# Optimization experiments

Hardware: AMD Instinct MI355X
Metric: run time of the kernel (lower is better)

Reference implementation:

```python
import jax, jax.numpy as jnp
import numpy as np

N_NODES = 50000
N_EDGES = 800000
NFEAT, NHID, NTOPIC = 256, 128, 64


def setup_inputs() -> dict:
    key = jax.random.key(0)
    k1, k2, k3, k4 = jax.random.split(key, 4)
    x = jax.random.normal(k1, (N_NODES, NFEAT), dtype=jnp.float32)
    edge_index = jax.random.randint(k2, (2, N_EDGES), 0, N_NODES, dtype=jnp.int64)
    W1 = jax.random.normal(k3, (NFEAT, NHID), dtype=jnp.float32) * (1.0 / np.sqrt(NFEAT))
    b1 = jnp.zeros((NHID,), dtype=jnp.float32)
    W2 = jax.random.normal(k4, (NHID, NTOPIC), dtype=jnp.float32) * (1.0 / np.sqrt(NHID))
    b2 = jnp.zeros((NTOPIC,), dtype=jnp.float32)
    return {"x": x, "edge_index": edge_index, "W1": W1, "b1": b1, "W2": W2, "b2": b2}


def reference(x, edge_index, W1, b1, W2, b2):
    # GCNConv (add_self_loops=False): symmetric normalization computed once (cached=True)
    n = x.shape[0]
    src, dst = edge_index[0], edge_index[1]
    deg = jnp.zeros((n,), dtype=x.dtype).at[dst].add(1.0)  # in-degree at targets
    deg_inv_sqrt = jnp.where(deg > 0, jax.lax.rsqrt(jnp.maximum(deg, 1.0)), 0.0)
    norm = deg_inv_sqrt[src] * deg_inv_sqrt[dst]  # [E]

    def gcn_conv(h, W, b):
        h = h @ W                                    # dense linear (bias=False)
        msg = norm[:, None] * h[src]                 # [E, out] edge messages
        agg = jax.ops.segment_sum(msg, dst, num_segments=n)
        return agg + b

    h = jax.nn.relu(gcn_conv(x, W1, b1))
    # dropout is identity in eval mode (train=False)
    return gcn_conv(h, W2, b2)
```

## Files before the change

kernel.cpp:

```cpp
#include <hip/hip_runtime.h>
#include <stdint.h>

#define NFEAT 256
#define NHID 128
#define NTOPIC 64
#define CAP 64

typedef __attribute__((ext_vector_type(8))) short bf16x8;
typedef __attribute__((ext_vector_type(4))) float f32x4;

__device__ inline float bf2f(unsigned int u16) {
    union { unsigned int i; float f; } v; v.i = u16 << 16; return v.f;
}
__device__ inline unsigned short f2bf(float f) {
    union { float f; unsigned int i; } v; v.f = f;
    unsigned int r = v.i + 0x7fff + ((v.i >> 16) & 1);
    return (unsigned short)(r >> 16);
}

__global__ void warm_kernel(const uint4* __restrict__ p, int total16) {
    int stride = gridDim.x * blockDim.x;
    unsigned acc = 0;
    for (int i = blockIdx.x * blockDim.x + threadIdx.x; i < total16; i += stride) {
        uint4 v = p[i];
        acc ^= v.x ^ v.y ^ v.z ^ v.w;
    }
    asm volatile("" :: "v"(acc));
}

__global__ void bucket_kernel(const int* __restrict__ src, const int* __restrict__ dst,
                              int* __restrict__ cnt, int* __restrict__ esrc_p, int E) {
    int e = blockIdx.x * blockDim.x + threadIdx.x;
    if (e < E) {
        int s = src[e], d = dst[e];
        int pos = atomicAdd(&cnt[d], 1);
        if (pos < CAP) esrc_p[(size_t)d * CAP + pos] = s;
    }
}

__global__ void castx_kernel(const float4* __restrict__ x4, const int* __restrict__ cnt,
                             ushort4* __restrict__ xb4, int total4) {
    int stride = gridDim.x * blockDim.x;
    for (int i = blockIdx.x * blockDim.x + threadIdx.x; i < total4; i += stride) {
        int c = cnt[i >> 6];
        float dn = (c > 0) ? rsqrtf((float)c) : 0.0f;
        float4 v = x4[i];
        ushort4 o;
        o.x = f2bf(dn * v.x); o.y = f2bf(dn * v.y);
        o.z = f2bf(dn * v.z); o.w = f2bf(dn * v.w);
        xb4[i] = o;
    }
}

__global__ void tw_kernel(const float* __restrict__ W, unsigned short* __restrict__ Wt,
                          int K, int N) {
    int idx = blockIdx.x * blockDim.x + threadIdx.x;
    if (idx < K * N) {
        int k = idx / N, c = idx - k * N;
        Wt[c * K + k] = f2bf(W[idx]);
    }
}

__global__ __launch_bounds__(256) void gemm1_mfma(const unsigned short* __restrict__ xb,
                                                  const unsigned short* __restrict__ Wt1,
                                                  unsigned short* __restrict__ h, int n) {
    int node0 = blockIdx.x * 16;
    int wave = threadIdx.x >> 6;
    int lane = threadIdx.x & 63;
    int r = lane & 15;
    int g = lane >> 4;
    int col0 = wave * 32;

    const unsigned short* arow  = xb  + (size_t)(node0 + r) * 256 + g * 8;
    const unsigned short* brow0 = Wt1 + (size_t)(col0 + r) * 256 + g * 8;
    const unsigned short* brow1 = Wt1 + (size_t)(col0 + 16 + r) * 256 + g * 8;

    f32x4 acc0 = {0.f, 0.f, 0.f, 0.f};
    f32x4 acc1 = {0.f, 0.f, 0.f, 0.f};
    #pragma unroll
    for (int k0 = 0; k0 < 256; k0 += 32) {
        bf16x8 a  = *(const bf16x8*)(arow + k0);
        bf16x8 b0 = *(const bf16x8*)(brow0 + k0);
        bf16x8 b1 = *(const bf16x8*)(brow1 + k0);
        acc0 = __builtin_amdgcn_mfma_f32_16x16x32_bf16(a, b0, acc0, 0, 0, 0);
        acc1 = __builtin_amdgcn_mfma_f32_16x16x32_bf16(a, b1, acc1, 0, 0, 0);
    }
    #pragma unroll
    for (int i = 0; i < 4; ++i) {
        int node = node0 + g * 4 + i;
        h[(size_t)node * 128 + col0 + r]      = f2bf(acc0[i]);
        h[(size_t)node * 128 + col0 + 16 + r] = f2bf(acc1[i]);
    }
}

__global__ __launch_bounds__(256) void gemm2_mfma(const unsigned short* __restrict__ agg1,
                                                  const unsigned short* __restrict__ Wt2,
                                                  unsigned short* __restrict__ h2, int n) {
    int node0 = blockIdx.x * 16;
    int wave = threadIdx.x >> 6;
    int lane = threadIdx.x & 63;
    int r = lane & 15;
    int g = lane >> 4;
    int col0 = wave * 16;

    const unsigned short* arow = agg1 + (size_t)(node0 + r) * 128 + g * 8;
    const unsigned short* brow = Wt2  + (size_t)(col0 + r) * 128 + g * 8;

    f32x4 acc = {0.f, 0.f, 0.f, 0.f};
    #pragma unroll
    for (int k0 = 0; k0 < 128; k0 += 32) {
        bf16x8 a = *(const bf16x8*)(arow + k0);
        bf16x8 b = *(const bf16x8*)(brow + k0);
        acc = __builtin_amdgcn_mfma_f32_16x16x32_bf16(a, b, acc, 0, 0, 0);
    }
    #pragma unroll
    for (int i = 0; i < 4; ++i) {
        int node = node0 + g * 4 + i;
        h2[(size_t)node * 64 + col0 + r] = f2bf(acc[i]);
    }
}

__global__ __launch_bounds__(256) void agg1_kernel(const int* __restrict__ cnt,
                                                   const int* __restrict__ esrc_p,
                                                   const unsigned short* __restrict__ h,
                                                   const float* __restrict__ bias,
                                                   unsigned short* __restrict__ agg, int n) {
    int wave = threadIdx.x >> 6;
    int lane = threadIdx.x & 63;
    int node = blockIdx.x * 4 + wave;
    if (node >= n) return;
    int c = cnt[node];
    float disn = (c > 0) ? rsqrtf((float)c) : 0.0f;
    int cntn = min(c, CAP);
    int g = lane >> 4;
    int r = lane & 15;
    const int* row = esrc_p + (size_t)node * CAP;
    const uint4* h4 = (const uint4*)h;

    float acc[8] = {0.f,0.f,0.f,0.f,0.f,0.f,0.f,0.f};
    for (int j = 0; j < cntn; j += 4) {
        int jj = j + g;
        if (jj < cntn) {
            int s = row[jj];
            uint4 hv = h4[(size_t)s * 16 + r];
            acc[0] += bf2f(hv.x & 0xffff); acc[1] += bf2f(hv.x >> 16);
            acc[2] += bf2f(hv.y & 0xffff); acc[3] += bf2f(hv.y >> 16);
            acc[4] += bf2f(hv.z & 0xffff); acc[5] += bf2f(hv.z >> 16);
            acc[6] += bf2f(hv.w & 0xffff); acc[7] += bf2f(hv.w >> 16);
        }
    }
    #pragma unroll
    for (int i = 0; i < 8; ++i) {
        acc[i] += __shfl_xor(acc[i], 16);
        acc[i] += __shfl_xor(acc[i], 32);
    }
    if (g == 0) {
        float4 b0 = ((const float4*)bias)[r * 2];
        float4 b1 = ((const float4*)bias)[r * 2 + 1];
        uint4 o;
        o.x = (unsigned)f2bf(disn * fmaxf(disn * acc[0] + b0.x, 0.f)) |
              ((unsigned)f2bf(disn * fmaxf(disn * acc[1] + b0.y, 0.f)) << 16);
        o.y = (unsigned)f2bf(disn * fmaxf(disn * acc[2] + b0.z, 0.f)) |
              ((unsigned)f2bf(disn * fmaxf(disn * acc[3] + b0.w, 0.f)) << 16);
        o.z = (unsigned)f2bf(disn * fmaxf(disn * acc[4] + b1.x, 0.f)) |
              ((unsigned)f2bf(disn * fmaxf(disn * acc[5] + b1.y, 0.f)) << 16);
        o.w = (unsigned)f2bf(disn * fmaxf(disn * acc[6] + b1.z, 0.f)) |
              ((unsigned)f2bf(disn * fmaxf(disn * acc[7] + b1.w, 0.f)) << 16);
        ((uint4*)agg)[(size_t)node * 16 + r] = o;
    }
}

__global__ __launch_bounds__(256) void agg2_kernel(const int* __restrict__ cnt,
                                                   const int* __restrict__ esrc_p,
                                                   const unsigned short* __restrict__ h2,
                                                   const float* __restrict__ bias,
                                                   float* __restrict__ out, int n) {
    int wave = threadIdx.x >> 6;
    int lane = threadIdx.x & 63;
    int node = blockIdx.x * 4 + wave;
    if (node >= n) return;
    int c = cnt[node];
    float disn = (c > 0) ? rsqrtf((float)c) : 0.0f;
    int cntn = min(c, CAP);
    int g = lane >> 4;
    int r = lane & 15;
    const int* row = esrc_p + (size_t)node * CAP;
    const uint2* h2v = (const uint2*)h2;

    float acc[4] = {0.f,0.f,0.f,0.f};
    for (int j = 0; j < cntn; j += 4) {
        int jj = j + g;
        if (jj < cntn) {
            int s = row[jj];
            uint2 hv = h2v[(size_t)s * 16 + r];
            acc[0] += bf2f(hv.x & 0xffff); acc[1] += bf2f(hv.x >> 16);
            acc[2] += bf2f(hv.y & 0xffff); acc[3] += bf2f(hv.y >> 16);
        }
    }
    #pragma unroll
    for (int i = 0; i < 4; ++i) {
        acc[i] += __shfl_xor(acc[i], 16);
        acc[i] += __shfl_xor(acc[i], 32);
    }
    if (g == 0) {
        float4 b = ((const float4*)bias)[r];
        float4 o;
        o.x = disn * acc[0] + b.x; o.y = disn * acc[1] + b.y;
        o.z = disn * acc[2] + b.z; o.w = disn * acc[3] + b.w;
        ((float4*)out)[(size_t)node * 16 + r] = o;
    }
}

extern "C" void kernel_launch(void* const* d_in, const int* in_sizes, int n_in,
                              void* d_out, int out_size, void* d_ws, size_t ws_size,
                              hipStream_t stream) {
    const float* x  = (const float*)d_in[0];
    const int*   ei = (const int*)d_in[1];
    const float* W1 = (const float*)d_in[2];
    const float* b1 = (const float*)d_in[3];
    const float* W2 = (const float*)d_in[4];
    const float* b2 = (const float*)d_in[5];
    float* out = (float*)d_out;

    const int n = in_sizes[0] / NFEAT;
    const int E = in_sizes[1] / 2;
    const int* src = ei;
    const int* dst = ei + E;

    const int n_al = (n + 63) & ~63;

    uintptr_t p = (uintptr_t)d_ws;
    auto take = [&p](size_t bytes) { uintptr_t r = p; p = (p + bytes + 15) & ~(uintptr_t)15; return r; };
    int*   esrc_p = (int*)take((size_t)n * CAP * 4);
    int*   cnt    = (int*)take((size_t)n_al * 4);
    unsigned short* Wt1  = (unsigned short*)take((size_t)NHID * NFEAT * 2);
    unsigned short* Wt2  = (unsigned short*)take((size_t)NTOPIC * NHID * 2);
    unsigned short* xb   = (unsigned short*)take((size_t)n * NFEAT * 2);
    unsigned short* h    = (unsigned short*)take((size_t)n * NHID * 2);
    unsigned short* agg1 = (unsigned short*)take((size_t)n * NHID * 2);

    hipMemsetAsync(cnt, 0, (size_t)n * sizeof(int), stream);
    warm_kernel<<<2048, 256, 0, stream>>>((const uint4*)esrc_p, n * CAP / 4);
    bucket_kernel<<<(E + 255) / 256, 256, 0, stream>>>(src, dst, cnt, esrc_p, E);

    castx_kernel<<<2048, 256, 0, stream>>>((const float4*)x, cnt, (ushort4*)xb, n * NFEAT / 4);
    tw_kernel<<<(NFEAT * NHID + 255) / 256, 256, 0, stream>>>(W1, Wt1, NFEAT, NHID);
    tw_kernel<<<(NHID * NTOPIC + 255) / 256, 256, 0, stream>>>(W2, Wt2, NHID, NTOPIC);

    gemm1_mfma<<<n / 16, 256, 0, stream>>>(xb, Wt1, h, n);
    agg1_kernel<<<(n + 3) / 4, 256, 0, stream>>>(cnt, esrc_p, h, b1, agg1, n);

    gemm2_mfma<<<n / 16, 256, 0, stream>>>(agg1, Wt2, h, n);
    agg2_kernel<<<(n + 3) / 4, 256, 0, stream>>>(cnt, esrc_p, h, b2, out, n);
}
```

Measured before the change: 272.6 us.

## Build padded adjacency via binned two-pass sort and fuse x cast into GEMM1

Replaces per-node global atomics with a bin histogram, scan, scatter into bins of 128 nodes, and a per-bin LDS pass that writes the padded adjacency with coalesced stores. Source indices are stored as 16-bit values, which halves adjacency traffic in the aggregation kernels. The separate cast-to-bf16 kernel and its buffer are removed; GEMM1 now reads fp32 x directly and scales and converts it in registers. In exchange this adds several launches and depends on node ids fitting in 16 bits (true for 50000 nodes).

```diff
diff --git a/kernel.cpp b/kernel.cpp
--- a/kernel.cpp
+++ b/kernel.cpp
@@ -5,6 +5,8 @@
 #define NHID 128
 #define NTOPIC 64
 #define CAP 64
+#define NPB 128
+#define NPB_SHIFT 7
 
 typedef __attribute__((ext_vector_type(8))) short bf16x8;
 typedef __attribute__((ext_vector_type(4))) float f32x4;
@@ -18,38 +20,73 @@
     return (unsigned short)(r >> 16);
 }
 
-__global__ void warm_kernel(const uint4* __restrict__ p, int total16) {
-    int stride = gridDim.x * blockDim.x;
-    unsigned acc = 0;
-    for (int i = blockIdx.x * blockDim.x + threadIdx.x; i < total16; i += stride) {
-        uint4 v = p[i];
-        acc ^= v.x ^ v.y ^ v.z ^ v.w;
-    }
-    asm volatile("" :: "v"(acc));
-}
-
-__global__ void bucket_kernel(const int* __restrict__ src, const int* __restrict__ dst,
-                              int* __restrict__ cnt, int* __restrict__ esrc_p, int E) {
+__global__ __launch_bounds__(256) void hist_kernel(const int* __restrict__ dst,
+                                                   int* __restrict__ binCnt, int E, int NB) {
+    __shared__ int lcnt[512];
+    for (int i = threadIdx.x; i < NB; i += 256) lcnt[i] = 0;
+    __syncthreads();
+    int stride = gridDim.x * 256;
+    for (int e = blockIdx.x * 256 + threadIdx.x; e < E; e += stride)
+        atomicAdd(&lcnt[dst[e] >> NPB_SHIFT], 1);
+    __syncthreads();
+    for (int i = threadIdx.x; i < NB; i += 256)
+        if (lcnt[i]) atomicAdd(&binCnt[i], lcnt[i]);
+}
+
+__global__ __launch_bounds__(512) void binscan_kernel(const int* __restrict__ binCnt,
+                                                      int* __restrict__ binptr,
+                                                      int* __restrict__ bincur, int NB) {
+    __shared__ int s[512];
+    int t = threadIdx.x;
+    s[t] = (t < NB) ? binCnt[t] : 0;
+    __syncthreads();
+    for (int off = 1; off < 512; off <<= 1) {
+        int v = (t >= off) ? s[t - off] : 0;
+        __syncthreads();
+        s[t] += v;
+        __syncthreads();
+    }
+    if (t < NB) {
+        int base = (t == 0) ? 0 : s[t - 1];
+        binptr[t] = base;
+        bincur[t] = base;
+        if (t == NB - 1) binptr[NB] = s[t];
+    }
+}
+
+__global__ void binscatter_kernel(const int* __restrict__ src, const int* __restrict__ dst,
+                                  int* __restrict__ bincur, unsigned* __restrict__ rec, int E) {
     int e = blockIdx.x * blockDim.x + threadIdx.x;
     if (e < E) {
-        int s = src[e], d = dst[e];
-        int pos = atomicAdd(&cnt[d], 1);
-        if (pos < CAP) esrc_p[(size_t)d * CAP + pos] = s;
-    }
-}
-
-__global__ void castx_kernel(const float4* __restrict__ x4, const int* __restrict__ cnt,
-                             ushort4* __restrict__ xb4, int total4) {
-    int stride = gridDim.x * blockDim.x;
-    for (int i = blockIdx.x * blockDim.x + threadIdx.x; i < total4; i += stride) {
-        int c = cnt[i >> 6];
-        float dn = (c > 0) ? rsqrtf((float)c) : 0.0f;
-        float4 v = x4[i];
-        ushort4 o;
-        o.x = f2bf(dn * v.x); o.y = f2bf(dn * v.y);
-        o.z = f2bf(dn * v.z); o.w = f2bf(dn * v.w);
-        xb4[i] = o;
-    }
+        int d = dst[e];
+        int b = d >> NPB_SHIFT;
+        int pos = atomicAdd(&bincur[b], 1);
+        rec[pos] = (unsigned)src[e] | ((unsigned)(d & (NPB - 1)) << 16);
+    }
+}
+
+__global__ __launch_bounds__(256) void csrbuild_kernel(const unsigned* __restrict__ rec,
+                                                       const int* __restrict__ binptr,
+                                                       unsigned short* __restrict__ esrc_p,
+                                                       int* __restrict__ cnt, int NB) {
+    __shared__ unsigned short lcsr[NPB * CAP];
+    __shared__ int lcnt[NPB];
+    int b = blockIdx.x;
+    for (int i = threadIdx.x; i < NPB; i += 256) lcnt[i] = 0;
+    __syncthreads();
+    int beg = binptr[b], end = binptr[b + 1];
+    for (int i = beg + threadIdx.x; i < end; i += 256) {
+        unsigned r = rec[i];
+        int dl = r >> 16;
+        int pos = atomicAdd(&lcnt[dl], 1);
+        if (pos < CAP) lcsr[dl * CAP + pos] = (unsigned short)(r & 0xffff);
+    }
+    __syncthreads();
+    uint4* gout = (uint4*)(esrc_p + (size_t)b * NPB * CAP);
+    const uint4* lin = (const uint4*)lcsr;
+    for (int i = threadIdx.x; i < NPB * CAP * 2 / 16; i += 256) gout[i] = lin[i];
+    int node0 = b * NPB;
+    for (int i = threadIdx.x; i < NPB; i += 256) cnt[node0 + i] = lcnt[i];
 }
 
 __global__ void tw_kernel(const float* __restrict__ W, unsigned short* __restrict__ Wt,
@@ -61,7 +98,8 @@
     }
 }
 
-__global__ __launch_bounds__(256) void gemm1_mfma(const unsigned short* __restrict__ xb,
+__global__ __launch_bounds__(256) void gemm1_mfma(const float* __restrict__ x,
+                                                  const int* __restrict__ cnt,
                                                   const unsigned short* __restrict__ Wt1,
                                                   unsigned short* __restrict__ h, int n) {
     int node0 = blockIdx.x * 16;
@@ -70,8 +108,11 @@
     int r = lane & 15;
     int g = lane >> 4;
     int col0 = wave * 32;
-
-    const unsigned short* arow  = xb  + (size_t)(node0 + r) * 256 + g * 8;
+    int row = node0 + r;
+
+    int c = cnt[row];
+    float dn = (c > 0) ? rsqrtf((float)c) : 0.0f;
+    const float* arow = x + (size_t)row * 256 + g * 8;
     const unsigned short* brow0 = Wt1 + (size_t)(col0 + r) * 256 + g * 8;
     const unsigned short* brow1 = Wt1 + (size_t)(col0 + 16 + r) * 256 + g * 8;
 
@@ -79,7 +120,13 @@
     f32x4 acc1 = {0.f, 0.f, 0.f, 0.f};
     #pragma unroll
     for (int k0 = 0; k0 < 256; k0 += 32) {
-        bf16x8 a  = *(const bf16x8*)(arow + k0);
+        float4 v0 = *(const float4*)(arow + k0);
+        float4 v1 = *(const float4*)(arow + k0 + 4);
+        bf16x8 a;
+        a[0] = (short)f2bf(dn * v0.x); a[1] = (short)f2bf(dn * v0.y);
+        a[2] = (short)f2bf(dn * v0.z); a[3] = (short)f2bf(dn * v0.w);
+        a[4] = (short)f2bf(dn * v1.x); a[5] = (short)f2bf(dn * v1.y);
+        a[6] = (short)f2bf(dn * v1.z); a[7] = (short)f2bf(dn * v1.w);
         bf16x8 b0 = *(const bf16x8*)(brow0 + k0);
         bf16x8 b1 = *(const bf16x8*)(brow1 + k0);
         acc0 = __builtin_amdgcn_mfma_f32_16x16x32_bf16(a, b0, acc0, 0, 0, 0);
@@ -121,7 +168,7 @@
 }
 
 __global__ __launch_bounds__(256) void agg1_kernel(const int* __restrict__ cnt,
-                                                   const int* __restrict__ esrc_p,
+                                                   const unsigned short* __restrict__ esrc_p,
                                                    const unsigned short* __restrict__ h,
                                                    const float* __restrict__ bias,
                                                    unsigned short* __restrict__ agg, int n) {
@@ -134,7 +181,7 @@
     int cntn = min(c, CAP);
     int g = lane >> 4;
     int r = lane & 15;
-    const int* row = esrc_p + (size_t)node * CAP;
+    const unsigned short* row = esrc_p + (size_t)node * CAP;
     const uint4* h4 = (const uint4*)h;
 
     float acc[8] = {0.f,0.f,0.f,0.f,0.f,0.f,0.f,0.f};
@@ -171,7 +218,7 @@
 }
 
 __global__ __launch_bounds__(256) void agg2_kernel(const int* __restrict__ cnt,
-                                                   const int* __restrict__ esrc_p,
+                                                   const unsigned short* __restrict__ esrc_p,
                                                    const unsigned short* __restrict__ h2,
                                                    const float* __restrict__ bias,
                                                    float* __restrict__ out, int n) {
@@ -184,7 +231,7 @@
     int cntn = min(c, CAP);
     int g = lane >> 4;
     int r = lane & 15;
-    const int* row = esrc_p + (size_t)node * CAP;
+    const unsigned short* row = esrc_p + (size_t)node * CAP;
     const uint2* h2v = (const uint2*)h2;
 
     float acc[4] = {0.f,0.f,0.f,0.f};
@@ -227,27 +274,32 @@
     const int* src = ei;
     const int* dst = ei + E;
 
-    const int n_al = (n + 63) & ~63;
+    const int NB = (n + NPB - 1) / NPB;
+    const int n_pad = NB * NPB;
 
     uintptr_t p = (uintptr_t)d_ws;
     auto take = [&p](size_t bytes) { uintptr_t r = p; p = (p + bytes + 15) & ~(uintptr_t)15; return r; };
-    int*   esrc_p = (int*)take((size_t)n * CAP * 4);
-    int*   cnt    = (int*)take((size_t)n_al * 4);
+    unsigned short* esrc_p = (unsigned short*)take((size_t)n_pad * CAP * 2);
+    unsigned* rec  = (unsigned*)take((size_t)E * 4);
+    int* cnt    = (int*)take((size_t)n_pad * 4);
+    int* binCnt = (int*)take((size_t)(NB + 1) * 4);
+    int* binptr = (int*)take((size_t)(NB + 1) * 4);
+    int* bincur = (int*)take((size_t)(NB + 1) * 4);
     unsigned short* Wt1  = (unsigned short*)take((size_t)NHID * NFEAT * 2);
     unsigned short* Wt2  = (unsigned short*)take((size_t)NTOPIC * NHID * 2);
-    unsigned short* xb   = (unsigned short*)take((size_t)n * NFEAT * 2);
     unsigned short* h    = (unsigned short*)take((size_t)n * NHID * 2);
     unsigned short* agg1 = (unsigned short*)take((size_t)n * NHID * 2);
 
-    hipMemsetAsync(cnt, 0, (size_t)n * sizeof(int), stream);
-    warm_kernel<<<2048, 256, 0, stream>>>((const uint4*)esrc_p, n * CAP / 4);
-    bucket_kernel<<<(E + 255) / 256, 256, 0, stream>>>(src, dst, cnt, esrc_p, E);
-
-    castx_kernel<<<2048, 256, 0, stream>>>((const float4*)x, cnt, (ushort4*)xb, n * NFEAT / 4);
+    hipMemsetAsync(binCnt, 0, (size_t)(NB + 1) * sizeof(int), stream);
+    hist_kernel<<<512, 256, 0, stream>>>(dst, binCnt, E, NB);
+    binscan_kernel<<<1, 512, 0, stream>>>(binCnt, binptr, bincur, NB);
+    binscatter_kernel<<<(E + 255) / 256, 256, 0, stream>>>(src, dst, bincur, rec, E);
+    csrbuild_kernel<<<NB, 256, 0, stream>>>(rec, binptr, esrc_p, cnt, NB);
+
     tw_kernel<<<(NFEAT * NHID + 255) / 256, 256, 0, stream>>>(W1, Wt1, NFEAT, NHID);
     tw_kernel<<<(NHID * NTOPIC + 255) / 256, 256, 0, stream>>>(W2, Wt2, NHID, NTOPIC);
 
-    gemm1_mfma<<<n / 16, 256, 0, stream>>>(xb, Wt1, h, n);
+    gemm1_mfma<<<n / 16, 256, 0, stream>>>(x, cnt, Wt1, h, n);
     agg1_kernel<<<(n + 3) / 4, 256, 0, stream>>>(cnt, esrc_p, h, b1, agg1, n);
 
     gemm2_mfma<<<n / 16, 256, 0, stream>>>(agg1, Wt2, h, n);
```

After: 537.4 us. 1.97x slower.

## Fuse x cast into GEMM1, pack edge indices as 16-bit, unroll gathers

Applied to the files above, without the earlier changes.

The separate castx pass is removed. GEMM1 now reads fp32 x directly and applies the degree scaling and bf16 conversion in registers, which avoids writing and re-reading a bf16 copy of x. Bucketed source indices are stored as 16-bit values packed with atomicOr into a zeroed buffer. This halves the index footprint read by both aggregation kernels and drops the warm-up kernel, at the cost of an extra memset and atomic ORs, and it only works while the node count fits in 16 bits. The aggregation loops now process two neighbour slots per iteration to raise memory-level parallelism.

```diff
diff --git a/kernel.cpp b/kernel.cpp
--- a/kernel.cpp
+++ b/kernel.cpp
@@ -18,37 +18,14 @@
     return (unsigned short)(r >> 16);
 }
 
-__global__ void warm_kernel(const uint4* __restrict__ p, int total16) {
-    int stride = gridDim.x * blockDim.x;
-    unsigned acc = 0;
-    for (int i = blockIdx.x * blockDim.x + threadIdx.x; i < total16; i += stride) {
-        uint4 v = p[i];
-        acc ^= v.x ^ v.y ^ v.z ^ v.w;
-    }
-    asm volatile("" :: "v"(acc));
-}
-
 __global__ void bucket_kernel(const int* __restrict__ src, const int* __restrict__ dst,
-                              int* __restrict__ cnt, int* __restrict__ esrc_p, int E) {
+                              int* __restrict__ cnt, unsigned* __restrict__ esrc_w, int E) {
     int e = blockIdx.x * blockDim.x + threadIdx.x;
     if (e < E) {
         int s = src[e], d = dst[e];
         int pos = atomicAdd(&cnt[d], 1);
-        if (pos < CAP) esrc_p[(size_t)d * CAP + pos] = s;
-    }
-}
-
-__global__ void castx_kernel(const float4* __restrict__ x4, const int* __restrict__ cnt,
-                             ushort4* __restrict__ xb4, int total4) {
-    int stride = gridDim.x * blockDim.x;
-    for (int i = blockIdx.x * blockDim.x + threadIdx.x; i < total4; i += stride) {
-        int c = cnt[i >> 6];
-        float dn = (c > 0) ? rsqrtf((float)c) : 0.0f;
-        float4 v = x4[i];
-        ushort4 o;
-        o.x = f2bf(dn * v.x); o.y = f2bf(dn * v.y);
-        o.z = f2bf(dn * v.z); o.w = f2bf(dn * v.w);
-        xb4[i] = o;
+        if (pos < CAP)
+            atomicOr(&esrc_w[d * (CAP / 2) + (pos >> 1)], ((unsigned)s) << ((pos & 1) * 16));
     }
 }
 
@@ -61,7 +38,8 @@
     }
 }
 
-__global__ __launch_bounds__(256) void gemm1_mfma(const unsigned short* __restrict__ xb,
+__global__ __launch_bounds__(256) void gemm1_mfma(const float* __restrict__ x,
+                                                  const int* __restrict__ cnt,
                                                   const unsigned short* __restrict__ Wt1,
                                                   unsigned short* __restrict__ h, int n) {
     int node0 = blockIdx.x * 16;
@@ -70,8 +48,11 @@
     int r = lane & 15;
     int g = lane >> 4;
     int col0 = wave * 32;
-
-    const unsigned short* arow  = xb  + (size_t)(node0 + r) * 256 + g * 8;
+    int row = node0 + r;
+
+    int c = cnt[row];
+    float dn = (c > 0) ? rsqrtf((float)c) : 0.0f;
+    const float* arow = x + (size_t)row * 256 + g * 8;
     const unsigned short* brow0 = Wt1 + (size_t)(col0 + r) * 256 + g * 8;
     const unsigned short* brow1 = Wt1 + (size_t)(col0 + 16 + r) * 256 + g * 8;
 
@@ -79,7 +60,13 @@
     f32x4 acc1 = {0.f, 0.f, 0.f, 0.f};
     #pragma unroll
     for (int k0 = 0; k0 < 256; k0 += 32) {
-        bf16x8 a  = *(const bf16x8*)(arow + k0);
+        float4 v0 = *(const float4*)(arow + k0);
+        float4 v1 = *(const float4*)(arow + k0 + 4);
+        bf16x8 a;
+        a[0] = (short)f2bf(dn * v0.x); a[1] = (short)f2bf(dn * v0.y);
+        a[2] = (short)f2bf(dn * v0.z); a[3] = (short)f2bf(dn * v0.w);
+        a[4] = (short)f2bf(dn * v1.x); a[5] = (short)f2bf(dn * v1.y);
+        a[6] = (short)f2bf(dn * v1.z); a[7] = (short)f2bf(dn * v1.w);
         bf16x8 b0 = *(const bf16x8*)(brow0 + k0);
         bf16x8 b1 = *(const bf16x8*)(brow1 + k0);
         acc0 = __builtin_amdgcn_mfma_f32_16x16x32_bf16(a, b0, acc0, 0, 0, 0);
@@ -121,7 +108,7 @@
 }
 
 __global__ __launch_bounds__(256) void agg1_kernel(const int* __restrict__ cnt,
-                                                   const int* __restrict__ esrc_p,
+                                                   const unsigned short* __restrict__ esrc_p,
                                                    const unsigned short* __restrict__ h,
                                                    const float* __restrict__ bias,
                                                    unsigned short* __restrict__ agg, int n) {
@@ -134,14 +121,23 @@
     int cntn = min(c, CAP);
     int g = lane >> 4;
     int r = lane & 15;
-    const int* row = esrc_p + (size_t)node * CAP;
+    const unsigned short* row = esrc_p + (size_t)node * CAP;
     const uint4* h4 = (const uint4*)h;
 
     float acc[8] = {0.f,0.f,0.f,0.f,0.f,0.f,0.f,0.f};
-    for (int j = 0; j < cntn; j += 4) {
-        int jj = j + g;
-        if (jj < cntn) {
-            int s = row[jj];
+    for (int j = 0; j < cntn; j += 8) {
+        int jj0 = j + g;
+        int jj1 = j + 4 + g;
+        if (jj0 < cntn) {
+            int s = row[jj0];
+            uint4 hv = h4[(size_t)s * 16 + r];
+            acc[0] += bf2f(hv.x & 0xffff); acc[1] += bf2f(hv.x >> 16);
+            acc[2] += bf2f(hv.y & 0xffff); acc[3] += bf2f(hv.y >> 16);
+            acc[4] += bf2f(hv.z & 0xffff); acc[5] += bf2f(hv.z >> 16);
+            acc[6] += bf2f(hv.w & 0xffff); acc[7] += bf2f(hv.w >> 16);
+        }
+        if (jj1 < cntn) {
+            int s = row[jj1];
             uint4 hv = h4[(size_t)s * 16 + r];
             acc[0] += bf2f(hv.x & 0xffff); acc[1] += bf2f(hv.x >> 16);
             acc[2] += bf2f(hv.y & 0xffff); acc[3] += bf2f(hv.y >> 16);
@@ -171,7 +167,7 @@
 }
 
 __global__ __launch_bounds__(256) void agg2_kernel(const int* __restrict__ cnt,
-                                                   const int* __restrict__ esrc_p,
+                                                   const unsigned short* __restrict__ esrc_p,
                                                    const unsigned short* __restrict__ h2,
                                                    const float* __restrict__ bias,
                                                    float* __restrict__ out, int n) {
@@ -184,14 +180,21 @@
     int cntn = min(c, CAP);
     int g = lane >> 4;
     int r = lane & 15;
-    const int* row = esrc_p + (size_t)node * CAP;
+    const unsigned short* row = esrc_p + (size_t)node * CAP;
     const uint2* h2v = (const uint2*)h2;
 
     float acc[4] = {0.f,0.f,0.f,0.f};
-    for (int j = 0; j < cntn; j += 4) {
-        int jj = j + g;
-        if (jj < cntn) {
-            int s = row[jj];
+    for (int j = 0; j < cntn; j += 8) {
+        int jj0 = j + g;
+        int jj1 = j + 4 + g;
+        if (jj0 < cntn) {
+            int s = row[jj0];
+            uint2 hv = h2v[(size_t)s * 16 + r];
+            acc[0] += bf2f(hv.x & 0xffff); acc[1] += bf2f(hv.x >> 16);
+            acc[2] += bf2f(hv.y & 0xffff); acc[3] += bf2f(hv.y >> 16);
+        }
+        if (jj1 < cntn) {
+            int s = row[jj1];
             uint2 hv = h2v[(size_t)s * 16 + r];
             acc[0] += bf2f(hv.x & 0xffff); acc[1] += bf2f(hv.x >> 16);
             acc[2] += bf2f(hv.y & 0xffff); acc[3] += bf2f(hv.y >> 16);
@@ -231,23 +234,21 @@
 
     uintptr_t p = (uintptr_t)d_ws;
     auto take = [&p](size_t bytes) { uintptr_t r = p; p = (p + bytes + 15) & ~(uintptr_t)15; return r; };
-    int*   esrc_p = (int*)take((size_t)n * CAP * 4);
-    int*   cnt    = (int*)take((size_t)n_al * 4);
+    unsigned short* esrc_p = (unsigned short*)take((size_t)n * CAP * 2);
+    int* cnt = (int*)take((size_t)n_al * 4);
     unsigned short* Wt1  = (unsigned short*)take((size_t)NHID * NFEAT * 2);
     unsigned short* Wt2  = (unsigned short*)take((size_t)NTOPIC * NHID * 2);
-    unsigned short* xb   = (unsigned short*)take((size_t)n * NFEAT * 2);
     unsigned short* h    = (unsigned short*)take((size_t)n * NHID * 2);
     unsigned short* agg1 = (unsigned short*)take((size_t)n * NHID * 2);
 
     hipMemsetAsync(cnt, 0, (size_t)n * sizeof(int), stream);
-    warm_kernel<<<2048, 256, 0, stream>>>((const uint4*)esrc_p, n * CAP / 4);
-    bucket_kernel<<<(E + 255) / 256, 256, 0, stream>>>(src, dst, cnt, esrc_p, E);
-
-    castx_kernel<<<2048, 256, 0, stream>>>((const float4*)x, cnt, (ushort4*)xb, n * NFEAT / 4);
+    hipMemsetAsync(esrc_p, 0, (size_t)n * CAP * 2, stream);
+    bucket_kernel<<<(E + 255) / 256, 256, 0, stream>>>(src, dst, cnt, (unsigned*)esrc_p, E);
+
     tw_kernel<<<(NFEAT * NHID + 255) / 256, 256, 0, stream>>>(W1, Wt1, NFEAT, NHID);
     tw_kernel<<<(NHID * NTOPIC + 255) / 256, 256, 0, stream>>>(W2, Wt2, NHID, NTOPIC);
 
-    gemm1_mfma<<<n / 16, 256, 0, stream>>>(xb, Wt1, h, n);
+    gemm1_mfma<<<n / 16, 256, 0, stream>>>(x, cnt, Wt1, h, n);
     agg1_kernel<<<(n + 3) / 4, 256, 0, stream>>>(cnt, esrc_p, h, b1, agg1, n);
 
     gemm2_mfma<<<n / 16, 256, 0, stream>>>(agg1, Wt2, h, n);
```

Measured after the change: 298.1 us. 9.3% more time.
